# Optimization experiments

Measured on AMD Instinct MI355X. Metric: run time of the kernel, lower is better.

## Reference

```python
import jax, jax.numpy as jnp
import numpy as np

N = 50000   # nodes
E = 800000  # edges per graph
FD = 128    # input feature dim (sc and fc)
H = 128     # hidden_dim
G = 64      # graphs in batch
C = 2       # num_classes


def _sage(x, src, dst, Wl, Wr, b, n):
    # PyG SAGEConv (mean aggr): lin_l(mean_{j->i} x_j) + lin_r(x_i); bias lives in lin_l.
    msum = jax.ops.segment_sum(x[src], dst, num_segments=n)          # [n, F]
    cnt = jax.ops.segment_sum(jnp.ones((src.shape[0],), x.dtype), dst, num_segments=n)
    mean = msum / jnp.maximum(cnt, 1.0)[:, None]
    return mean @ Wl.T + x @ Wr.T + b


def setup_inputs() -> dict:
    key = jax.random.key(0)
    ks = jax.random.split(key, 24)
    s = 0.05
    inp = {
        "sc_x": jax.random.normal(ks[0], (N, FD), jnp.float32),
        "fc_x": jax.random.normal(ks[1], (N, FD), jnp.float32),
        "sc_edge_index": jax.random.randint(ks[2], (2, E), 0, N),
        "fc_edge_index": jax.random.randint(ks[3], (2, E), 0, N),
        "batch": jnp.sort(jax.random.randint(ks[4], (N,), 0, G)),
        # sc convs
        "sc_Wl1": jax.random.normal(ks[5], (H, FD), jnp.float32) * s,
        "sc_Wr1": jax.random.normal(ks[6], (H, FD), jnp.float32) * s,
        "sc_b1": jnp.zeros((H,), jnp.float32),
        "sc_Wl2": jax.random.normal(ks[7], (H, H), jnp.float32) * s,
        "sc_Wr2": jax.random.normal(ks[8], (H, H), jnp.float32) * s,
        "sc_b2": jnp.zeros((H,), jnp.float32),
        # fc convs
        "fc_Wl1": jax.random.normal(ks[9], (H, FD), jnp.float32) * s,
        "fc_Wr1": jax.random.normal(ks[10], (H, FD), jnp.float32) * s,
        "fc_b1": jnp.zeros((H,), jnp.float32),
        "fc_Wl2": jax.random.normal(ks[11], (H, H), jnp.float32) * s,
        "fc_Wr2": jax.random.normal(ks[12], (H, H), jnp.float32) * s,
        "fc_b2": jnp.zeros((H,), jnp.float32),
        # MLP head
        "W1": jax.random.normal(ks[13], (H, 2 * H), jnp.float32) * s,
        "bh1": jnp.zeros((H,), jnp.float32),
        "W2": jax.random.normal(ks[14], (H // 2, H), jnp.float32) * s,
        "bh2": jnp.zeros((H // 2,), jnp.float32),
        "W3": jax.random.normal(ks[15], (C, H // 2), jnp.float32) * s,
        "bh3": jnp.zeros((C,), jnp.float32),
    }
    return inp


def reference(sc_x, fc_x, sc_edge_index, fc_edge_index, batch,
              sc_Wl1, sc_Wr1, sc_b1, sc_Wl2, sc_Wr2, sc_b2,
              fc_Wl1, fc_Wr1, fc_b1, fc_Wl2, fc_Wr2, fc_b2,
              W1, bh1, W2, bh2, W3, bh3):
    # edge_index[0] = source j, edge_index[1] = target i (PyG convention)
    sc_src, sc_dst = sc_edge_index[0], sc_edge_index[1]
    fc_src, fc_dst = fc_edge_index[0], fc_edge_index[1]

    h = jax.nn.relu(_sage(sc_x, sc_src, sc_dst, sc_Wl1, sc_Wr1, sc_b1, N))
    h = jax.nn.relu(_sage(h, sc_src, sc_dst, sc_Wl2, sc_Wr2, sc_b2, N))
    sc_pool = jax.ops.segment_sum(h, batch, num_segments=G)  # global_add_pool -> [G, H]

    g = jax.nn.relu(_sage(fc_x, fc_src, fc_dst, fc_Wl1, fc_Wr1, fc_b1, N))
    g = jax.nn.relu(_sage(g, fc_src, fc_dst, fc_Wl2, fc_Wr2, fc_b2, N))
    fc_pool = jax.ops.segment_sum(g, batch, num_segments=G)  # [G, H]

    x = jnp.concatenate([sc_pool, fc_pool], axis=1)          # [G, 2H]
    # dropout is identity in eval mode
    x = jax.nn.relu(x @ W1.T + bh1)
    x = jax.nn.relu(x @ W2.T + bh2)
    return jax.nn.log_softmax(x @ W3.T + bh3, axis=-1)       # [G, C]
```

## Files before the change

### kernel.cpp

```cpp
#include <hip/hip_runtime.h>
#include <hip/hip_bf16.h>

#define N_NODES 50000
#define E_EDGES 800000
#define G_GRAPHS 64
#define NBUCK 392
#define BCAP 5120
#define NF ((size_t)N_NODES * 128)

typedef __attribute__((ext_vector_type(8))) short s16x8;
typedef __attribute__((ext_vector_type(4))) float f32x4;

constexpr size_t O_POOL   = 0;
constexpr size_t O_GCUR   = 16384;
constexpr size_t O_ROW    = 17408;
constexpr size_t O_CNT    = 117408;
constexpr size_t O_ES     = 217408;
constexpr size_t O_WB     = 1817408;
constexpr size_t O_XB     = 1882944;
constexpr size_t O_MEAN   = 8282944;
constexpr size_t O_HB     = 14682944;
constexpr size_t ZERO_BYTES = (16384 + 512) * 4;

__device__ __forceinline__ unsigned short f2bf(float f) {
    __hip_bfloat16 h = __float2bfloat16(f);
    return *reinterpret_cast<unsigned short*>(&h);
}
__device__ __forceinline__ float bflo(unsigned int v) { return __uint_as_float(v << 16); }
__device__ __forceinline__ float bfhi(unsigned int v) { return __uint_as_float(v & 0xffff0000u); }

__global__ void __launch_bounds__(512) bin_pass1(const int* __restrict__ sc_e,
                                                 const int* __restrict__ fc_e,
                                                 int* __restrict__ gcur,
                                                 unsigned int* __restrict__ buf) {
    __shared__ int hcnt[512];
    __shared__ int hexcl[512];
    __shared__ int hcur[512];
    __shared__ int gbase[512];
    __shared__ int wsum[8];
    __shared__ unsigned int stage[4096];

    const int tid = threadIdx.x;
    const int lane = tid & 63;
    const int wid = tid >> 6;
    const int tile0 = blockIdx.x * 4096;

    hcnt[tid] = 0;
    __syncthreads();

    int eb[8];
    unsigned int pk[8];
    #pragma unroll
    for (int j = 0; j < 8; ++j) {
        int ec = tile0 + j * 512 + tid;
        if (ec < 2 * E_EDGES) {
            int set = (ec >= E_EDGES);
            int local = ec - set * E_EDGES;
            const int* ep = set ? fc_e : sc_e;
            int src = ep[local];
            int dst = ep[E_EDGES + local];
            eb[j] = set * 196 + (dst >> 8);
            pk[j] = ((unsigned int)(dst & 255) << 16) | (unsigned int)src;
            atomicAdd(&hcnt[eb[j]], 1);
        } else eb[j] = -1;
    }
    __syncthreads();

    {
        int v = hcnt[tid];
        int incl = v;
        #pragma unroll
        for (int d = 1; d < 64; d <<= 1) {
            int u = __shfl_up(incl, d, 64);
            if (lane >= d) incl += u;
        }
        if (lane == 63) wsum[wid] = incl;
        __syncthreads();
        int pre = 0;
        for (int w = 0; w < wid; ++w) pre += wsum[w];
        int excl = incl - v + pre;
        hexcl[tid] = excl;
        hcur[tid] = excl;
    }
    __syncthreads();

    if (tid < NBUCK) {
        int c = hcnt[tid];
        gbase[tid] = c ? atomicAdd(&gcur[tid], c) : 0;
    }

    #pragma unroll
    for (int j = 0; j < 8; ++j) {
        if (eb[j] >= 0) {
            int pos = atomicAdd(&hcur[eb[j]], 1);
            stage[pos] = pk[j];
        }
    }
    __syncthreads();

    for (int b = wid; b < NBUCK; b += 8) {
        int c = hcnt[b];
        if (!c) continue;
        int s = hexcl[b];
        int g0 = gbase[b];
        for (int i = lane; i < c; i += 64) {
            int gi = g0 + i;
            if (gi < BCAP) buf[(size_t)b * BCAP + gi] = stage[s + i];
        }
    }
}

__global__ void __launch_bounds__(256) bin_pass2(const unsigned int* __restrict__ buf,
                                                 const int* __restrict__ gcur,
                                                 int* __restrict__ row,
                                                 int* __restrict__ cnt,
                                                 int* __restrict__ es) {
    __shared__ int cntl[256];
    __shared__ int pexcl[256];
    __shared__ int pcur[256];
    __shared__ int wsum[4];
    __shared__ int pre[512];
    __shared__ int stage[BCAP];

    const int b = blockIdx.x;
    const int tid = threadIdx.x;
    const int lane = tid & 63, wid = tid >> 6;
    const int sz = min(gcur[b], BCAP);
    const unsigned int* mybuf = buf + (size_t)b * BCAP;
    const int n0 = (b % 196) * 256;
    const int setbase = (b / 196) * N_NODES;

    pre[tid] = (tid < NBUCK) ? min(gcur[tid], BCAP) : 0;
    if (tid + 256 < 512) pre[tid + 256] = (tid + 256 < NBUCK) ? min(gcur[tid + 256], BCAP) : 0;
    cntl[tid] = 0;
    __syncthreads();
    if (tid < 64) {
        int base = tid * 8;
        int loc[8];
        int s = 0;
        #pragma unroll
        for (int k = 0; k < 8; ++k) { loc[k] = s; s += pre[base + k]; }
        int incl = s;
        #pragma unroll
        for (int d = 1; d < 64; d <<= 1) {
            int u = __shfl_up(incl, d, 64);
            if (lane >= d) incl += u;
        }
        int excl = incl - s;
        #pragma unroll
        for (int k = 0; k < 8; ++k) pre[base + k] = excl + loc[k];
    }
    for (int i = tid; i < sz; i += 256)
        atomicAdd(&cntl[mybuf[i] >> 16], 1);
    __syncthreads();
    const int base = pre[b];
    {
        int v = cntl[tid];
        int incl = v;
        #pragma unroll
        for (int d = 1; d < 64; d <<= 1) {
            int u = __shfl_up(incl, d, 64);
            if (lane >= d) incl += u;
        }
        if (lane == 63) wsum[wid] = incl;
        __syncthreads();
        int p = 0;
        for (int w = 0; w < wid; ++w) p += wsum[w];
        int excl = incl - v + p;
        pexcl[tid] = excl;
        pcur[tid] = excl;
    }
    __syncthreads();
    for (int i = tid; i < sz; i += 256) {
        unsigned int p = mybuf[i];
        int pos = atomicAdd(&pcur[p >> 16], 1);
        stage[pos] = (int)(p & 0xFFFFu);
    }
    __syncthreads();
    for (int i = tid; i < sz; i += 256) es[base + i] = stage[i];
    int node = n0 + tid;
    if (node < N_NODES) {
        cnt[setbase + node] = cntl[tid];
        row[setbase + node] = base + pexcl[tid];
    }
}

__global__ void cvt_all(const float* __restrict__ sc_x, const float* __restrict__ fc_x,
                        const float* w0, const float* w1, const float* w2, const float* w3,
                        const float* w4, const float* w5, const float* w6, const float* w7,
                        unsigned short* __restrict__ xb, unsigned short* __restrict__ wb) {
    const int blk = blockIdx.x;
    const int tid = threadIdx.x;
    if (blk < 6250) {
        int i = blk * 256 + tid;
        int set = (i >= (N_NODES * 128) / 8);
        int local = i - set * (N_NODES * 128) / 8;
        const float* src = set ? fc_x : sc_x;
        const float4* s = reinterpret_cast<const float4*>(src) + (size_t)local * 2;
        float4 a = s[0], b = s[1];
        union { s16x8 v; unsigned short u[8]; } p;
        p.u[0] = f2bf(a.x); p.u[1] = f2bf(a.y); p.u[2] = f2bf(a.z); p.u[3] = f2bf(a.w);
        p.u[4] = f2bf(b.x); p.u[5] = f2bf(b.y); p.u[6] = f2bf(b.z); p.u[7] = f2bf(b.w);
        reinterpret_cast<s16x8*>(xb)[i] = p.v;
    } else {
        int widx = blk - 6250;
        int gi = widx * 2048 + tid * 8;
        int m = gi >> 14;
        int off = gi & 16383;
        const float* W;
        switch (m) {
            case 0: W = w0; break; case 1: W = w1; break;
            case 2: W = w2; break; case 3: W = w3; break;
            case 4: W = w4; break; case 5: W = w5; break;
            case 6: W = w6; break; default: W = w7; break;
        }
        const float4* s = reinterpret_cast<const float4*>(W + off);
        float4 a = s[0], b = s[1];
        union { s16x8 v; unsigned short u[8]; } p;
        p.u[0] = f2bf(a.x); p.u[1] = f2bf(a.y); p.u[2] = f2bf(a.z); p.u[3] = f2bf(a.w);
        p.u[4] = f2bf(b.x); p.u[5] = f2bf(b.y); p.u[6] = f2bf(b.z); p.u[7] = f2bf(b.w);
        *reinterpret_cast<s16x8*>(wb + gi) = p.v;
    }
}

__global__ void __launch_bounds__(256) agg_kernel(const unsigned short* __restrict__ x,
                                                  const int* __restrict__ row,
                                                  const int* __restrict__ cnt,
                                                  const int* __restrict__ es,
                                                  unsigned short* __restrict__ mean) {
    int wave = (blockIdx.x * 256 + threadIdx.x) >> 6;
    int lane = threadIdx.x & 63;
    int ql = lane & 15;
    int n = wave * 4 + (lane >> 4);
    if (n >= 2 * N_NODES) return;
    const unsigned short* xs = x + (n >= N_NODES ? NF : 0);
    int start = row[n];
    int deg = cnt[n];
    float a0 = 0.f, a1 = 0.f, a2 = 0.f, a3 = 0.f, a4 = 0.f, a5 = 0.f, a6 = 0.f, a7 = 0.f;
    int qbase = lane & 48;
    for (int c = 0; c < deg; c += 16) {
        int m = min(16, deg - c);
        int eid = (ql < m) ? es[start + c + ql] : 0;
        int j = 0;
        for (; j + 4 <= m; j += 4) {
            int s0 = __shfl(eid, qbase + j,     64);
            int s1 = __shfl(eid, qbase + j + 1, 64);
            int s2 = __shfl(eid, qbase + j + 2, 64);
            int s3 = __shfl(eid, qbase + j + 3, 64);
            uint4 v0 = *reinterpret_cast<const uint4*>(xs + (size_t)s0 * 128 + ql * 8);
            uint4 v1 = *reinterpret_cast<const uint4*>(xs + (size_t)s1 * 128 + ql * 8);
            uint4 v2 = *reinterpret_cast<const uint4*>(xs + (size_t)s2 * 128 + ql * 8);
            uint4 v3 = *reinterpret_cast<const uint4*>(xs + (size_t)s3 * 128 + ql * 8);
            a0 += bflo(v0.x) + bflo(v1.x) + bflo(v2.x) + bflo(v3.x);
            a1 += bfhi(v0.x) + bfhi(v1.x) + bfhi(v2.x) + bfhi(v3.x);
            a2 += bflo(v0.y) + bflo(v1.y) + bflo(v2.y) + bflo(v3.y);
            a3 += bfhi(v0.y) + bfhi(v1.y) + bfhi(v2.y) + bfhi(v3.y);
            a4 += bflo(v0.z) + bflo(v1.z) + bflo(v2.z) + bflo(v3.z);
            a5 += bfhi(v0.z) + bfhi(v1.z) + bfhi(v2.z) + bfhi(v3.z);
            a6 += bflo(v0.w) + bflo(v1.w) + bflo(v2.w) + bflo(v3.w);
            a7 += bfhi(v0.w) + bfhi(v1.w) + bfhi(v2.w) + bfhi(v3.w);
        }
        for (; j < m; ++j) {
            int s = __shfl(eid, qbase + j, 64);
            uint4 v = *reinterpret_cast<const uint4*>(xs + (size_t)s * 128 + ql * 8);
            a0 += bflo(v.x); a1 += bfhi(v.x);
            a2 += bflo(v.y); a3 += bfhi(v.y);
            a4 += bflo(v.z); a5 += bfhi(v.z);
            a6 += bflo(v.w); a7 += bfhi(v.w);
        }
    }
    float inv = 1.0f / fmaxf((float)deg, 1.0f);
    uint4 o;
    o.x = (unsigned int)f2bf(a0 * inv) | ((unsigned int)f2bf(a1 * inv) << 16);
    o.y = (unsigned int)f2bf(a2 * inv) | ((unsigned int)f2bf(a3 * inv) << 16);
    o.z = (unsigned int)f2bf(a4 * inv) | ((unsigned int)f2bf(a5 * inv) << 16);
    o.w = (unsigned int)f2bf(a6 * inv) | ((unsigned int)f2bf(a7 * inv) << 16);
    *reinterpret_cast<uint4*>(mean + (size_t)n * 128 + ql * 8) = o;
}

__global__ void __launch_bounds__(512) gemm_mfma(const unsigned short* __restrict__ AmB,
                                                 const unsigned short* __restrict__ AxB,
                                                 const unsigned short* __restrict__ WBall,
                                                 const float* __restrict__ bias0,
                                                 const float* __restrict__ bias1,
                                                 unsigned short* __restrict__ outHB,
                                                 float* __restrict__ pool,
                                                 const int* __restrict__ batch,
                                                 int layer) {
    __shared__ s16x8 lds_a[2][512];
    __shared__ s16x8 lds_b[2][512];

    const int tid = threadIdx.x;
    const int lane = tid & 63;
    const int w = tid >> 6;
    const int set = blockIdx.y;
    const int node0 = blockIdx.x * 128;

    const unsigned short* Am = AmB + (size_t)set * NF;
    const unsigned short* Ax = AxB + (size_t)set * NF;
    const unsigned short* Bl = WBall + (size_t)(set * 4 + layer * 2) * 16384;
    const unsigned short* Br = Bl + 16384;
    const float* bias = set ? bias1 : bias0;
    unsigned short* outH = outHB ? outHB + (size_t)set * NF : nullptr;
    const int poolBase = set * 128;

    const int wr = w >> 1;
    const int wc = w & 1;
    const int fr = lane & 15;
    const int fg = lane >> 4;

    f32x4 acc[2][4];
    #pragma unroll
    for (int mf = 0; mf < 2; ++mf)
        #pragma unroll
        for (int nf = 0; nf < 4; ++nf) acc[mf][nf] = (f32x4){0.f, 0.f, 0.f, 0.f};

    const int s_row = tid >> 2, s_slot = tid & 3;
    const int s_g = s_slot ^ ((s_row >> 1) & 3);
    const size_t a_off = (size_t)min(node0 + s_row, N_NODES - 1) * 128 + s_g * 8;
    const size_t b_off = (size_t)s_row * 128 + s_g * 8;

    const int arow0 = wr * 32 + fr;
    const int arow1 = arow0 + 16;
    const int aidx0 = arow0 * 4 + (fg ^ ((arow0 >> 1) & 3));
    const int aidx1 = arow1 * 4 + (fg ^ ((arow1 >> 1) & 3));
    int bidx[4];
    #pragma unroll
    for (int nf = 0; nf < 4; ++nf) {
        int br = wc * 64 + nf * 16 + fr;
        bidx[nf] = br * 4 + (fg ^ ((br >> 1) & 3));
    }

    #define LOAD_A(kc) (*reinterpret_cast<const s16x8*>(((kc) < 4 ? Am : Ax) + (((kc) & 3) * 32) + a_off))
    #define LOAD_B(kc) (*reinterpret_cast<const s16x8*>(((kc) < 4 ? Bl : Br) + (((kc) & 3) * 32) + b_off))

    {
        s16x8 ra = LOAD_A(0), rb = LOAD_B(0);
        lds_a[0][tid] = ra; lds_b[0][tid] = rb;
    }
    __syncthreads();

    #pragma unroll
    for (int kc = 0; kc < 8; ++kc) {
        const int cur = kc & 1;
        s16x8 ra, rb;
        if (kc < 7) { ra = LOAD_A(kc + 1); rb = LOAD_B(kc + 1); }
        s16x8 a0 = lds_a[cur][aidx0];
        s16x8 a1 = lds_a[cur][aidx1];
        #pragma unroll
        for (int nf = 0; nf < 4; ++nf) {
            s16x8 bv = lds_b[cur][bidx[nf]];
            acc[0][nf] = __builtin_amdgcn_mfma_f32_16x16x32_bf16(a0, bv, acc[0][nf], 0, 0, 0);
            acc[1][nf] = __builtin_amdgcn_mfma_f32_16x16x32_bf16(a1, bv, acc[1][nf], 0, 0, 0);
        }
        if (kc < 7) { lds_a[cur ^ 1][tid] = ra; lds_b[cur ^ 1][tid] = rb; }
        __syncthreads();
    }
    #undef LOAD_A
    #undef LOAD_B

    if (outH) {
        #pragma unroll
        for (int mf = 0; mf < 2; ++mf)
            #pragma unroll
            for (int nf = 0; nf < 4; ++nf) {
                int col = wc * 64 + nf * 16 + fr;
                float bv = bias[col];
                #pragma unroll
                for (int r = 0; r < 4; ++r) {
                    int node = node0 + wr * 32 + mf * 16 + fg * 4 + r;
                    if (node < N_NODES)
                        outH[(size_t)node * 128 + col] = f2bf(fmaxf(acc[mf][nf][r] + bv, 0.f));
                }
            }
    } else {
        int gids[2][4];
        #pragma unroll
        for (int mf = 0; mf < 2; ++mf)
            #pragma unroll
            for (int r = 0; r < 4; ++r) {
                int node = node0 + wr * 32 + mf * 16 + fg * 4 + r;
                gids[mf][r] = (node < N_NODES) ? batch[node] : -1;
            }
        #pragma unroll
        for (int nf = 0; nf < 4; ++nf) {
            int col = wc * 64 + nf * 16 + fr;
            float bv = bias[col];
            float* pbase = &pool[poolBase + col];
            int curg = -1; float s = 0.f;
            #pragma unroll
            for (int mf = 0; mf < 2; ++mf)
                #pragma unroll
                for (int r = 0; r < 4; ++r) {
                    int g = gids[mf][r];
                    if (g < 0) continue;
                    float v = fmaxf(acc[mf][nf][r] + bv, 0.f);
                    if (g != curg) {
                        if (curg >= 0) atomicAdd(pbase + (size_t)curg * 256, s);
                        curg = g; s = v;
                    } else s += v;
                }
            if (curg >= 0) atomicAdd(pbase + (size_t)curg * 256, s);
        }
    }
}

__global__ void __launch_bounds__(128) head_kernel(const float* __restrict__ pool,
                                                   const float* __restrict__ W1, const float* __restrict__ bh1,
                                                   const float* __restrict__ W2, const float* __restrict__ bh2,
                                                   const float* __restrict__ W3, const float* __restrict__ bh3,
                                                   float* __restrict__ out) {
    __shared__ float xg[256];
    __shared__ float h1[128];
    __shared__ float h2[64];
    __shared__ float lg[2];
    int g = blockIdx.x, t = threadIdx.x;
    xg[t] = pool[(size_t)g * 256 + t];
    xg[t + 128] = pool[(size_t)g * 256 + 128 + t];
    __syncthreads();
    float s = bh1[t];
    for (int k = 0; k < 256; ++k) s += W1[t * 256 + k] * xg[k];
    h1[t] = fmaxf(s, 0.f);
    __syncthreads();
    if (t < 64) {
        float s2 = bh2[t];
        for (int k = 0; k < 128; ++k) s2 += W2[t * 128 + k] * h1[k];
        h2[t] = fmaxf(s2, 0.f);
    }
    __syncthreads();
    if (t < 2) {
        float s3 = bh3[t];
        for (int k = 0; k < 64; ++k) s3 += W3[t * 64 + k] * h2[k];
        lg[t] = s3;
    }
    __syncthreads();
    if (t == 0) {
        float m = fmaxf(lg[0], lg[1]);
        float lse = m + logf(expf(lg[0] - m) + expf(lg[1] - m));
        out[g * 2 + 0] = lg[0] - lse;
        out[g * 2 + 1] = lg[1] - lse;
    }
}

extern "C" void kernel_launch(void* const* d_in, const int* in_sizes, int n_in,
                              void* d_out, int out_size, void* d_ws, size_t ws_size,
                              hipStream_t stream) {
    const float* sc_x = (const float*)d_in[0];
    const float* fc_x = (const float*)d_in[1];
    const int* sc_e   = (const int*)d_in[2];
    const int* fc_e   = (const int*)d_in[3];
    const int* batch  = (const int*)d_in[4];
    const float* sc_Wl1 = (const float*)d_in[5];
    const float* sc_Wr1 = (const float*)d_in[6];
    const float* sc_b1  = (const float*)d_in[7];
    const float* sc_Wl2 = (const float*)d_in[8];
    const float* sc_Wr2 = (const float*)d_in[9];
    const float* sc_b2  = (const float*)d_in[10];
    const float* fc_Wl1 = (const float*)d_in[11];
    const float* fc_Wr1 = (const float*)d_in[12];
    const float* fc_b1  = (const float*)d_in[13];
    const float* fc_Wl2 = (const float*)d_in[14];
    const float* fc_Wr2 = (const float*)d_in[15];
    const float* fc_b2  = (const float*)d_in[16];
    const float* W1  = (const float*)d_in[17];
    const float* bh1 = (const float*)d_in[18];
    const float* W2  = (const float*)d_in[19];
    const float* bh2 = (const float*)d_in[20];
    const float* W3  = (const float*)d_in[21];
    const float* bh3 = (const float*)d_in[22];

    int* iw = (int*)d_ws;
    float* fw = (float*)d_ws;
    float* pool = fw + O_POOL;
    int* gcur   = iw + O_GCUR;
    int* row    = iw + O_ROW;
    int* cnt    = iw + O_CNT;
    int* es     = iw + O_ES;
    unsigned short* WB    = (unsigned short*)(iw + O_WB);
    unsigned short* xb    = (unsigned short*)(iw + O_XB);
    unsigned short* meanb = (unsigned short*)(iw + O_MEAN);
    unsigned short* hb    = (unsigned short*)(iw + O_HB);
    unsigned int* buf = (unsigned int*)(iw + O_MEAN);

    hipMemsetAsync(d_ws, 0, ZERO_BYTES, stream);

    bin_pass1<<<(2 * E_EDGES + 4095) / 4096, 512, 0, stream>>>(sc_e, fc_e, gcur, buf);
    bin_pass2<<<NBUCK, 256, 0, stream>>>(buf, gcur, row, cnt, es);

    cvt_all<<<6250 + 64, 256, 0, stream>>>(sc_x, fc_x,
                                           sc_Wl1, sc_Wr1, sc_Wl2, sc_Wr2,
                                           fc_Wl1, fc_Wr1, fc_Wl2, fc_Wr2, xb, WB);

    const int AGB = (2 * N_NODES + 15) / 16;
    dim3 gg((N_NODES + 127) / 128, 2);

    agg_kernel<<<AGB, 256, 0, stream>>>(xb, row, cnt, es, meanb);
    gemm_mfma<<<gg, 512, 0, stream>>>(meanb, xb, WB, sc_b1, fc_b1, hb, nullptr, nullptr, 0);
    agg_kernel<<<AGB, 256, 0, stream>>>(hb, row, cnt, es, meanb);
    gemm_mfma<<<gg, 512, 0, stream>>>(meanb, hb, WB, sc_b2, fc_b2, nullptr, pool, batch, 1);

    head_kernel<<<G_GRAPHS, 128, 0, stream>>>(pool, W1, bh1, W2, bh2, W3, bh3, (float*)d_out);
}
```

Measured before the change: 342.7 us.

## Fuse neighbor mean aggregation into SAGE MFMA GEMM kernel via LDS

Merges the separate aggregation kernel and the GEMM kernel into one kernel per layer. Each block computes the neighbor means for 64 nodes directly into shared memory and then runs the bf16 MFMA GEMM on them, so the mean matrix never makes a round trip through global memory and two launches per forward are removed. In exchange the tile shrinks to 64 nodes (more blocks, each wave covering fewer output columns), and the irregular gather now shares a block with the GEMM, which may lower occupancy and MFMA utilization.

```diff
diff --git a/kernel.cpp b/kernel.cpp
--- a/kernel.cpp
+++ b/kernel.cpp
@@ -18,7 +18,7 @@
 constexpr size_t O_ES     = 217408;
 constexpr size_t O_WB     = 1817408;
 constexpr size_t O_XB     = 1882944;
-constexpr size_t O_MEAN   = 8282944;
+constexpr size_t O_BUF    = 8282944;
 constexpr size_t O_HB     = 14682944;
 constexpr size_t ZERO_BYTES = (16384 + 512) * 4;
 
@@ -223,148 +223,154 @@
     }
 }
 
-__global__ void __launch_bounds__(256) agg_kernel(const unsigned short* __restrict__ x,
+__global__ void __launch_bounds__(512) sage_fused(const unsigned short* __restrict__ xAll,
+                                                  const unsigned short* __restrict__ WBall,
                                                   const int* __restrict__ row,
                                                   const int* __restrict__ cnt,
                                                   const int* __restrict__ es,
-                                                  unsigned short* __restrict__ mean) {
-    int wave = (blockIdx.x * 256 + threadIdx.x) >> 6;
-    int lane = threadIdx.x & 63;
-    int ql = lane & 15;
-    int n = wave * 4 + (lane >> 4);
-    if (n >= 2 * N_NODES) return;
-    const unsigned short* xs = x + (n >= N_NODES ? NF : 0);
-    int start = row[n];
-    int deg = cnt[n];
-    float a0 = 0.f, a1 = 0.f, a2 = 0.f, a3 = 0.f, a4 = 0.f, a5 = 0.f, a6 = 0.f, a7 = 0.f;
-    int qbase = lane & 48;
-    for (int c = 0; c < deg; c += 16) {
-        int m = min(16, deg - c);
-        int eid = (ql < m) ? es[start + c + ql] : 0;
-        int j = 0;
-        for (; j + 4 <= m; j += 4) {
-            int s0 = __shfl(eid, qbase + j,     64);
-            int s1 = __shfl(eid, qbase + j + 1, 64);
-            int s2 = __shfl(eid, qbase + j + 2, 64);
-            int s3 = __shfl(eid, qbase + j + 3, 64);
-            uint4 v0 = *reinterpret_cast<const uint4*>(xs + (size_t)s0 * 128 + ql * 8);
-            uint4 v1 = *reinterpret_cast<const uint4*>(xs + (size_t)s1 * 128 + ql * 8);
-            uint4 v2 = *reinterpret_cast<const uint4*>(xs + (size_t)s2 * 128 + ql * 8);
-            uint4 v3 = *reinterpret_cast<const uint4*>(xs + (size_t)s3 * 128 + ql * 8);
-            a0 += bflo(v0.x) + bflo(v1.x) + bflo(v2.x) + bflo(v3.x);
-            a1 += bfhi(v0.x) + bfhi(v1.x) + bfhi(v2.x) + bfhi(v3.x);
-            a2 += bflo(v0.y) + bflo(v1.y) + bflo(v2.y) + bflo(v3.y);
-            a3 += bfhi(v0.y) + bfhi(v1.y) + bfhi(v2.y) + bfhi(v3.y);
-            a4 += bflo(v0.z) + bflo(v1.z) + bflo(v2.z) + bflo(v3.z);
-            a5 += bfhi(v0.z) + bfhi(v1.z) + bfhi(v2.z) + bfhi(v3.z);
-            a6 += bflo(v0.w) + bflo(v1.w) + bflo(v2.w) + bflo(v3.w);
-            a7 += bfhi(v0.w) + bfhi(v1.w) + bfhi(v2.w) + bfhi(v3.w);
-        }
-        for (; j < m; ++j) {
-            int s = __shfl(eid, qbase + j, 64);
-            uint4 v = *reinterpret_cast<const uint4*>(xs + (size_t)s * 128 + ql * 8);
-            a0 += bflo(v.x); a1 += bfhi(v.x);
-            a2 += bflo(v.y); a3 += bfhi(v.y);
-            a4 += bflo(v.z); a5 += bfhi(v.z);
-            a6 += bflo(v.w); a7 += bfhi(v.w);
-        }
-    }
-    float inv = 1.0f / fmaxf((float)deg, 1.0f);
-    uint4 o;
-    o.x = (unsigned int)f2bf(a0 * inv) | ((unsigned int)f2bf(a1 * inv) << 16);
-    o.y = (unsigned int)f2bf(a2 * inv) | ((unsigned int)f2bf(a3 * inv) << 16);
-    o.z = (unsigned int)f2bf(a4 * inv) | ((unsigned int)f2bf(a5 * inv) << 16);
-    o.w = (unsigned int)f2bf(a6 * inv) | ((unsigned int)f2bf(a7 * inv) << 16);
-    *reinterpret_cast<uint4*>(mean + (size_t)n * 128 + ql * 8) = o;
-}
-
-__global__ void __launch_bounds__(512) gemm_mfma(const unsigned short* __restrict__ AmB,
-                                                 const unsigned short* __restrict__ AxB,
-                                                 const unsigned short* __restrict__ WBall,
-                                                 const float* __restrict__ bias0,
-                                                 const float* __restrict__ bias1,
-                                                 unsigned short* __restrict__ outHB,
-                                                 float* __restrict__ pool,
-                                                 const int* __restrict__ batch,
-                                                 int layer) {
-    __shared__ s16x8 lds_a[2][512];
+                                                  const float* __restrict__ bias0,
+                                                  const float* __restrict__ bias1,
+                                                  unsigned short* __restrict__ outHB,
+                                                  float* __restrict__ pool,
+                                                  const int* __restrict__ batch,
+                                                  int layer) {
+    __shared__ s16x8 mean_t[64 * 17];
+    __shared__ s16x8 lds_a[2][256];
     __shared__ s16x8 lds_b[2][512];
 
     const int tid = threadIdx.x;
     const int lane = tid & 63;
     const int w = tid >> 6;
     const int set = blockIdx.y;
-    const int node0 = blockIdx.x * 128;
-
-    const unsigned short* Am = AmB + (size_t)set * NF;
-    const unsigned short* Ax = AxB + (size_t)set * NF;
+    const int node0 = blockIdx.x * 64;
+    const int setbase = set * N_NODES;
+
+    const unsigned short* xs = xAll + (size_t)set * NF;
     const unsigned short* Bl = WBall + (size_t)(set * 4 + layer * 2) * 16384;
     const unsigned short* Br = Bl + 16384;
     const float* bias = set ? bias1 : bias0;
     unsigned short* outH = outHB ? outHB + (size_t)set * NF : nullptr;
     const int poolBase = set * 128;
 
-    const int wr = w >> 1;
-    const int wc = w & 1;
+    const int s_row = tid >> 2, s_slot = tid & 3;
+    const int s_g = s_slot ^ ((s_row >> 1) & 3);
+    const size_t b_off = (size_t)s_row * 128 + s_g * 8;
+    const size_t a_off = (size_t)min(node0 + s_row, N_NODES - 1) * 128 + s_g * 8;
+
+    #define LOAD_AX(kc) (*reinterpret_cast<const s16x8*>(xs + (((kc) & 3) * 32) + a_off))
+    #define LOAD_B(kc)  (*reinterpret_cast<const s16x8*>(((kc) < 4 ? Bl : Br) + (((kc) & 3) * 32) + b_off))
+
+    s16x8 rb0 = LOAD_B(0);
+
+    const int ql = lane & 15;
+    const int q = lane >> 4;
+    const int qbase = lane & 48;
+    #pragma unroll
+    for (int pass = 0; pass < 2; ++pass) {
+        int r = pass * 32 + w * 4 + q;
+        int n = node0 + r;
+        int deg = (n < N_NODES) ? cnt[setbase + n] : 0;
+        int start = (n < N_NODES) ? row[setbase + n] : 0;
+        float a0 = 0.f, a1 = 0.f, a2 = 0.f, a3 = 0.f, a4 = 0.f, a5 = 0.f, a6 = 0.f, a7 = 0.f;
+        for (int c = 0; c < deg; c += 16) {
+            int m = min(16, deg - c);
+            int eid = (ql < m) ? es[start + c + ql] : 0;
+            int j = 0;
+            for (; j + 4 <= m; j += 4) {
+                int s0 = __shfl(eid, qbase + j,     64);
+                int s1 = __shfl(eid, qbase + j + 1, 64);
+                int s2 = __shfl(eid, qbase + j + 2, 64);
+                int s3 = __shfl(eid, qbase + j + 3, 64);
+                uint4 v0 = *reinterpret_cast<const uint4*>(xs + (size_t)s0 * 128 + ql * 8);
+                uint4 v1 = *reinterpret_cast<const uint4*>(xs + (size_t)s1 * 128 + ql * 8);
+                uint4 v2 = *reinterpret_cast<const uint4*>(xs + (size_t)s2 * 128 + ql * 8);
+                uint4 v3 = *reinterpret_cast<const uint4*>(xs + (size_t)s3 * 128 + ql * 8);
+                a0 += bflo(v0.x) + bflo(v1.x) + bflo(v2.x) + bflo(v3.x);
+                a1 += bfhi(v0.x) + bfhi(v1.x) + bfhi(v2.x) + bfhi(v3.x);
+                a2 += bflo(v0.y) + bflo(v1.y) + bflo(v2.y) + bflo(v3.y);
+                a3 += bfhi(v0.y) + bfhi(v1.y) + bfhi(v2.y) + bfhi(v3.y);
+                a4 += bflo(v0.z) + bflo(v1.z) + bflo(v2.z) + bflo(v3.z);
+                a5 += bfhi(v0.z) + bfhi(v1.z) + bfhi(v2.z) + bfhi(v3.z);
+                a6 += bflo(v0.w) + bflo(v1.w) + bflo(v2.w) + bflo(v3.w);
+                a7 += bfhi(v0.w) + bfhi(v1.w) + bfhi(v2.w) + bfhi(v3.w);
+            }
+            for (; j < m; ++j) {
+                int s = __shfl(eid, qbase + j, 64);
+                uint4 v = *reinterpret_cast<const uint4*>(xs + (size_t)s * 128 + ql * 8);
+                a0 += bflo(v.x); a1 += bfhi(v.x);
+                a2 += bflo(v.y); a3 += bfhi(v.y);
+                a4 += bflo(v.z); a5 += bfhi(v.z);
+                a6 += bflo(v.w); a7 += bfhi(v.w);
+            }
+        }
+        float inv = 1.0f / fmaxf((float)deg, 1.0f);
+        union { s16x8 v; unsigned int u[4]; } o;
+        o.u[0] = (unsigned int)f2bf(a0 * inv) | ((unsigned int)f2bf(a1 * inv) << 16);
+        o.u[1] = (unsigned int)f2bf(a2 * inv) | ((unsigned int)f2bf(a3 * inv) << 16);
+        o.u[2] = (unsigned int)f2bf(a4 * inv) | ((unsigned int)f2bf(a5 * inv) << 16);
+        o.u[3] = (unsigned int)f2bf(a6 * inv) | ((unsigned int)f2bf(a7 * inv) << 16);
+        mean_t[r * 17 + ql] = o.v;
+    }
+    lds_b[0][tid] = rb0;
+    __syncthreads();
+
+    const int wr = w >> 2;
+    const int wc = w & 3;
     const int fr = lane & 15;
     const int fg = lane >> 4;
 
-    f32x4 acc[2][4];
+    f32x4 acc[2][2];
     #pragma unroll
     for (int mf = 0; mf < 2; ++mf)
         #pragma unroll
-        for (int nf = 0; nf < 4; ++nf) acc[mf][nf] = (f32x4){0.f, 0.f, 0.f, 0.f};
-
-    const int s_row = tid >> 2, s_slot = tid & 3;
-    const int s_g = s_slot ^ ((s_row >> 1) & 3);
-    const size_t a_off = (size_t)min(node0 + s_row, N_NODES - 1) * 128 + s_g * 8;
-    const size_t b_off = (size_t)s_row * 128 + s_g * 8;
+        for (int nf = 0; nf < 2; ++nf) acc[mf][nf] = (f32x4){0.f, 0.f, 0.f, 0.f};
 
     const int arow0 = wr * 32 + fr;
     const int arow1 = arow0 + 16;
-    const int aidx0 = arow0 * 4 + (fg ^ ((arow0 >> 1) & 3));
-    const int aidx1 = arow1 * 4 + (fg ^ ((arow1 >> 1) & 3));
-    int bidx[4];
+    const int axidx0 = arow0 * 4 + (fg ^ ((arow0 >> 1) & 3));
+    const int axidx1 = arow1 * 4 + (fg ^ ((arow1 >> 1) & 3));
+    int bidx[2];
     #pragma unroll
-    for (int nf = 0; nf < 4; ++nf) {
-        int br = wc * 64 + nf * 16 + fr;
-        bidx[nf] = br * 4 + (fg ^ ((br >> 1) & 3));
-    }
-
-    #define LOAD_A(kc) (*reinterpret_cast<const s16x8*>(((kc) < 4 ? Am : Ax) + (((kc) & 3) * 32) + a_off))
-    #define LOAD_B(kc) (*reinterpret_cast<const s16x8*>(((kc) < 4 ? Bl : Br) + (((kc) & 3) * 32) + b_off))
-
-    {
-        s16x8 ra = LOAD_A(0), rb = LOAD_B(0);
-        lds_a[0][tid] = ra; lds_b[0][tid] = rb;
-    }
-    __syncthreads();
+    for (int nf = 0; nf < 2; ++nf) {
+        int brr = wc * 32 + nf * 16 + fr;
+        bidx[nf] = brr * 4 + (fg ^ ((brr >> 1) & 3));
+    }
 
     #pragma unroll
     for (int kc = 0; kc < 8; ++kc) {
         const int cur = kc & 1;
-        s16x8 ra, rb;
-        if (kc < 7) { ra = LOAD_A(kc + 1); rb = LOAD_B(kc + 1); }
-        s16x8 a0 = lds_a[cur][aidx0];
-        s16x8 a1 = lds_a[cur][aidx1];
-        #pragma unroll
-        for (int nf = 0; nf < 4; ++nf) {
+        s16x8 rbn, ran;
+        if (kc < 7) rbn = LOAD_B(kc + 1);
+        if (kc >= 3 && kc < 7 && tid < 256) ran = LOAD_AX(kc + 1);
+        s16x8 a0, a1;
+        if (kc < 4) {
+            a0 = mean_t[arow0 * 17 + kc * 4 + fg];
+            a1 = mean_t[arow1 * 17 + kc * 4 + fg];
+        } else {
+            a0 = lds_a[cur][axidx0];
+            a1 = lds_a[cur][axidx1];
+        }
+        #pragma unroll
+        for (int nf = 0; nf < 2; ++nf) {
             s16x8 bv = lds_b[cur][bidx[nf]];
             acc[0][nf] = __builtin_amdgcn_mfma_f32_16x16x32_bf16(a0, bv, acc[0][nf], 0, 0, 0);
             acc[1][nf] = __builtin_amdgcn_mfma_f32_16x16x32_bf16(a1, bv, acc[1][nf], 0, 0, 0);
         }
-        if (kc < 7) { lds_a[cur ^ 1][tid] = ra; lds_b[cur ^ 1][tid] = rb; }
+        if (kc < 7) {
+            lds_b[cur ^ 1][tid] = rbn;
+            if (kc >= 3 && tid < 256) lds_a[(kc + 1) & 1][tid] = ran;
+        }
         __syncthreads();
     }
-    #undef LOAD_A
+    #undef LOAD_AX
     #undef LOAD_B
 
     if (outH) {
         #pragma unroll
         for (int mf = 0; mf < 2; ++mf)
             #pragma unroll
-            for (int nf = 0; nf < 4; ++nf) {
-                int col = wc * 64 + nf * 16 + fr;
+            for (int nf = 0; nf < 2; ++nf) {
+                int col = wc * 32 + nf * 16 + fr;
                 float bv = bias[col];
                 #pragma unroll
                 for (int r = 0; r < 4; ++r) {
@@ -383,8 +389,8 @@
                 gids[mf][r] = (node < N_NODES) ? batch[node] : -1;
             }
         #pragma unroll
-        for (int nf = 0; nf < 4; ++nf) {
-            int col = wc * 64 + nf * 16 + fr;
+        for (int nf = 0; nf < 2; ++nf) {
+            int col = wc * 32 + nf * 16 + fr;
             float bv = bias[col];
             float* pbase = &pool[poolBase + col];
             int curg = -1; float s = 0.f;
@@ -476,11 +482,10 @@
     int* row    = iw + O_ROW;
     int* cnt    = iw + O_CNT;
     int* es     = iw + O_ES;
-    unsigned short* WB    = (unsigned short*)(iw + O_WB);
-    unsigned short* xb    = (unsigned short*)(iw + O_XB);
-    unsigned short* meanb = (unsigned short*)(iw + O_MEAN);
-    unsigned short* hb    = (unsigned short*)(iw + O_HB);
-    unsigned int* buf = (unsigned int*)(iw + O_MEAN);
+    unsigned short* WB = (unsigned short*)(iw + O_WB);
+    unsigned short* xb = (unsigned short*)(iw + O_XB);
+    unsigned short* hb = (unsigned short*)(iw + O_HB);
+    unsigned int* buf  = (unsigned int*)(iw + O_BUF);
 
     hipMemsetAsync(d_ws, 0, ZERO_BYTES, stream);
 
@@ -491,13 +496,10 @@
                                            sc_Wl1, sc_Wr1, sc_Wl2, sc_Wr2,
                                            fc_Wl1, fc_Wr1, fc_Wl2, fc_Wr2, xb, WB);
 
-    const int AGB = (2 * N_NODES + 15) / 16;
-    dim3 gg((N_NODES + 127) / 128, 2);
-
-    agg_kernel<<<AGB, 256, 0, stream>>>(xb, row, cnt, es, meanb);
-    gemm_mfma<<<gg, 512, 0, stream>>>(meanb, xb, WB, sc_b1, fc_b1, hb, nullptr, nullptr, 0);
-    agg_kernel<<<AGB, 256, 0, stream>>>(hb, row, cnt, es, meanb);
-    gemm_mfma<<<gg, 512, 0, stream>>>(meanb, hb, WB, sc_b2, fc_b2, nullptr, pool, batch, 1);
+    dim3 gf((N_NODES + 63) / 64, 2);
+
+    sage_fused<<<gf, 512, 0, stream>>>(xb, WB, row, cnt, es, sc_b1, fc_b1, hb, nullptr, nullptr, 0);
+    sage_fused<<<gf, 512, 0, stream>>>(hb, WB, row, cnt, es, sc_b2, fc_b2, nullptr, pool, batch, 1);
 
     head_kernel<<<G_GRAPHS, 128, 0, stream>>>(pool, W1, bh1, W2, bh2, W3, bh3, (float*)d_out);
 }
```

Measured after the change: 346.3 us. Within noise of the previous version (+1.0%).

## Fuse binning, conversion and pool zeroing into one prep kernel with per-tile slots

Applied to the files above, without the earlier changes.

Merges the first binning pass, the feature and weight bf16 conversion, and the pool zeroing into a single launch, which removes the memset and one kernel launch. Global atomic bucket cursors are replaced by fixed per-(bucket, tile) slots with capacity TCAP plus a count array. The second pass prefix-sums those per-tile counts and gathers the slots into shared memory, and es now uses fixed per-bucket offsets. The cost is a larger scratch buffer and a serial per-thread gather loop in the second pass. Any tile contributing more than TCAP edges to one bucket is silently truncated.

```diff
diff --git a/kernel.cpp b/kernel.cpp
--- a/kernel.cpp
+++ b/kernel.cpp
@@ -5,22 +5,24 @@
 #define E_EDGES 800000
 #define G_GRAPHS 64
 #define NBUCK 392
+#define NTILE 391
+#define TCAP 40
 #define BCAP 5120
 #define NF ((size_t)N_NODES * 128)
 
 typedef __attribute__((ext_vector_type(8))) short s16x8;
 typedef __attribute__((ext_vector_type(4))) float f32x4;
 
-constexpr size_t O_POOL   = 0;
-constexpr size_t O_GCUR   = 16384;
-constexpr size_t O_ROW    = 17408;
-constexpr size_t O_CNT    = 117408;
-constexpr size_t O_ES     = 217408;
-constexpr size_t O_WB     = 1817408;
-constexpr size_t O_XB     = 1882944;
-constexpr size_t O_MEAN   = 8282944;
-constexpr size_t O_HB     = 14682944;
-constexpr size_t ZERO_BYTES = (16384 + 512) * 4;
+constexpr size_t O_POOL = 0;
+constexpr size_t O_ROW  = 16384;
+constexpr size_t O_CNT  = 116384;
+constexpr size_t O_ES   = 216384;
+constexpr size_t O_TCNT = 2223424;
+constexpr size_t O_WB   = 2376704;
+constexpr size_t O_XB   = 2442240;
+constexpr size_t O_MEAN = 8842240;
+constexpr size_t O_HB   = 15242240;
+constexpr size_t O_BUF  = 21642240;
 
 __device__ __forceinline__ unsigned short f2bf(float f) {
     __hip_bfloat16 h = __float2bfloat16(f);
@@ -29,172 +31,92 @@
 __device__ __forceinline__ float bflo(unsigned int v) { return __uint_as_float(v << 16); }
 __device__ __forceinline__ float bfhi(unsigned int v) { return __uint_as_float(v & 0xffff0000u); }
 
-__global__ void __launch_bounds__(512) bin_pass1(const int* __restrict__ sc_e,
-                                                 const int* __restrict__ fc_e,
-                                                 int* __restrict__ gcur,
-                                                 unsigned int* __restrict__ buf) {
+__global__ void __launch_bounds__(512) prep_kernel(const int* __restrict__ sc_e,
+                                                   const int* __restrict__ fc_e,
+                                                   const float* __restrict__ sc_x,
+                                                   const float* __restrict__ fc_x,
+                                                   const float* w0, const float* w1,
+                                                   const float* w2, const float* w3,
+                                                   const float* w4, const float* w5,
+                                                   const float* w6, const float* w7,
+                                                   unsigned int* __restrict__ buf,
+                                                   int* __restrict__ tcnt,
+                                                   unsigned short* __restrict__ xb,
+                                                   unsigned short* __restrict__ wb,
+                                                   float* __restrict__ pool) {
     __shared__ int hcnt[512];
     __shared__ int hexcl[512];
     __shared__ int hcur[512];
-    __shared__ int gbase[512];
     __shared__ int wsum[8];
     __shared__ unsigned int stage[4096];
 
-    const int tid = threadIdx.x;
-    const int lane = tid & 63;
-    const int wid = tid >> 6;
-    const int tile0 = blockIdx.x * 4096;
-
-    hcnt[tid] = 0;
-    __syncthreads();
-
-    int eb[8];
-    unsigned int pk[8];
-    #pragma unroll
-    for (int j = 0; j < 8; ++j) {
-        int ec = tile0 + j * 512 + tid;
-        if (ec < 2 * E_EDGES) {
-            int set = (ec >= E_EDGES);
-            int local = ec - set * E_EDGES;
-            const int* ep = set ? fc_e : sc_e;
-            int src = ep[local];
-            int dst = ep[E_EDGES + local];
-            eb[j] = set * 196 + (dst >> 8);
-            pk[j] = ((unsigned int)(dst & 255) << 16) | (unsigned int)src;
-            atomicAdd(&hcnt[eb[j]], 1);
-        } else eb[j] = -1;
-    }
-    __syncthreads();
-
-    {
-        int v = hcnt[tid];
-        int incl = v;
-        #pragma unroll
-        for (int d = 1; d < 64; d <<= 1) {
-            int u = __shfl_up(incl, d, 64);
-            if (lane >= d) incl += u;
-        }
-        if (lane == 63) wsum[wid] = incl;
-        __syncthreads();
-        int pre = 0;
-        for (int w = 0; w < wid; ++w) pre += wsum[w];
-        int excl = incl - v + pre;
-        hexcl[tid] = excl;
-        hcur[tid] = excl;
-    }
-    __syncthreads();
-
-    if (tid < NBUCK) {
-        int c = hcnt[tid];
-        gbase[tid] = c ? atomicAdd(&gcur[tid], c) : 0;
-    }
-
-    #pragma unroll
-    for (int j = 0; j < 8; ++j) {
-        if (eb[j] >= 0) {
-            int pos = atomicAdd(&hcur[eb[j]], 1);
-            stage[pos] = pk[j];
-        }
-    }
-    __syncthreads();
-
-    for (int b = wid; b < NBUCK; b += 8) {
-        int c = hcnt[b];
-        if (!c) continue;
-        int s = hexcl[b];
-        int g0 = gbase[b];
-        for (int i = lane; i < c; i += 64) {
-            int gi = g0 + i;
-            if (gi < BCAP) buf[(size_t)b * BCAP + gi] = stage[s + i];
-        }
-    }
-}
-
-__global__ void __launch_bounds__(256) bin_pass2(const unsigned int* __restrict__ buf,
-                                                 const int* __restrict__ gcur,
-                                                 int* __restrict__ row,
-                                                 int* __restrict__ cnt,
-                                                 int* __restrict__ es) {
-    __shared__ int cntl[256];
-    __shared__ int pexcl[256];
-    __shared__ int pcur[256];
-    __shared__ int wsum[4];
-    __shared__ int pre[512];
-    __shared__ int stage[BCAP];
-
-    const int b = blockIdx.x;
-    const int tid = threadIdx.x;
-    const int lane = tid & 63, wid = tid >> 6;
-    const int sz = min(gcur[b], BCAP);
-    const unsigned int* mybuf = buf + (size_t)b * BCAP;
-    const int n0 = (b % 196) * 256;
-    const int setbase = (b / 196) * N_NODES;
-
-    pre[tid] = (tid < NBUCK) ? min(gcur[tid], BCAP) : 0;
-    if (tid + 256 < 512) pre[tid + 256] = (tid + 256 < NBUCK) ? min(gcur[tid + 256], BCAP) : 0;
-    cntl[tid] = 0;
-    __syncthreads();
-    if (tid < 64) {
-        int base = tid * 8;
-        int loc[8];
-        int s = 0;
-        #pragma unroll
-        for (int k = 0; k < 8; ++k) { loc[k] = s; s += pre[base + k]; }
-        int incl = s;
-        #pragma unroll
-        for (int d = 1; d < 64; d <<= 1) {
-            int u = __shfl_up(incl, d, 64);
-            if (lane >= d) incl += u;
-        }
-        int excl = incl - s;
-        #pragma unroll
-        for (int k = 0; k < 8; ++k) pre[base + k] = excl + loc[k];
-    }
-    for (int i = tid; i < sz; i += 256)
-        atomicAdd(&cntl[mybuf[i] >> 16], 1);
-    __syncthreads();
-    const int base = pre[b];
-    {
-        int v = cntl[tid];
-        int incl = v;
-        #pragma unroll
-        for (int d = 1; d < 64; d <<= 1) {
-            int u = __shfl_up(incl, d, 64);
-            if (lane >= d) incl += u;
-        }
-        if (lane == 63) wsum[wid] = incl;
-        __syncthreads();
-        int p = 0;
-        for (int w = 0; w < wid; ++w) p += wsum[w];
-        int excl = incl - v + p;
-        pexcl[tid] = excl;
-        pcur[tid] = excl;
-    }
-    __syncthreads();
-    for (int i = tid; i < sz; i += 256) {
-        unsigned int p = mybuf[i];
-        int pos = atomicAdd(&pcur[p >> 16], 1);
-        stage[pos] = (int)(p & 0xFFFFu);
-    }
-    __syncthreads();
-    for (int i = tid; i < sz; i += 256) es[base + i] = stage[i];
-    int node = n0 + tid;
-    if (node < N_NODES) {
-        cnt[setbase + node] = cntl[tid];
-        row[setbase + node] = base + pexcl[tid];
-    }
-}
-
-__global__ void cvt_all(const float* __restrict__ sc_x, const float* __restrict__ fc_x,
-                        const float* w0, const float* w1, const float* w2, const float* w3,
-                        const float* w4, const float* w5, const float* w6, const float* w7,
-                        unsigned short* __restrict__ xb, unsigned short* __restrict__ wb) {
     const int blk = blockIdx.x;
     const int tid = threadIdx.x;
-    if (blk < 6250) {
-        int i = blk * 256 + tid;
-        int set = (i >= (N_NODES * 128) / 8);
-        int local = i - set * (N_NODES * 128) / 8;
+
+    if (blk < NTILE) {
+        const int lane = tid & 63;
+        const int wid = tid >> 6;
+        const int tile0 = blk * 4096;
+
+        hcnt[tid] = 0;
+        __syncthreads();
+
+        int eb[8];
+        unsigned int pk[8];
+        #pragma unroll
+        for (int j = 0; j < 8; ++j) {
+            int ec = tile0 + j * 512 + tid;
+            if (ec < 2 * E_EDGES) {
+                int set = (ec >= E_EDGES);
+                int local = ec - set * E_EDGES;
+                const int* ep = set ? fc_e : sc_e;
+                int src = ep[local];
+                int dst = ep[E_EDGES + local];
+                eb[j] = set * 196 + (dst >> 8);
+                pk[j] = ((unsigned int)(dst & 255) << 16) | (unsigned int)src;
+                atomicAdd(&hcnt[eb[j]], 1);
+            } else eb[j] = -1;
+        }
+        __syncthreads();
+
+        {
+            int v = hcnt[tid];
+            int incl = v;
+            #pragma unroll
+            for (int d = 1; d < 64; d <<= 1) {
+                int u = __shfl_up(incl, d, 64);
+                if (lane >= d) incl += u;
+            }
+            if (lane == 63) wsum[wid] = incl;
+            __syncthreads();
+            int pre = 0;
+            for (int w = 0; w < wid; ++w) pre += wsum[w];
+            int excl = incl - v + pre;
+            hexcl[tid] = excl;
+            hcur[tid] = excl;
+        }
+        __syncthreads();
+
+        #pragma unroll
+        for (int j = 0; j < 8; ++j) {
+            if (eb[j] >= 0) {
+                int pos = atomicAdd(&hcur[eb[j]], 1);
+                stage[pos] = pk[j];
+            }
+        }
+        __syncthreads();
+
+        for (int b = wid; b < NBUCK; b += 8) {
+            int c = min(hcnt[b], TCAP);
+            int s = hexcl[b];
+            size_t g0 = ((size_t)b * NTILE + blk) * TCAP;
+            for (int i = lane; i < c; i += 64) buf[g0 + i] = stage[s + i];
+            if (lane == 0) tcnt[b * NTILE + blk] = c;
+        }
+    } else if (blk < NTILE + 3125) {
+        int i = (blk - NTILE) * 512 + tid;
+        int set = (i >= 800000);
+        int local = i - set * 800000;
         const float* src = set ? fc_x : sc_x;
         const float4* s = reinterpret_cast<const float4*>(src) + (size_t)local * 2;
         float4 a = s[0], b = s[1];
@@ -202,9 +124,9 @@
         p.u[0] = f2bf(a.x); p.u[1] = f2bf(a.y); p.u[2] = f2bf(a.z); p.u[3] = f2bf(a.w);
         p.u[4] = f2bf(b.x); p.u[5] = f2bf(b.y); p.u[6] = f2bf(b.z); p.u[7] = f2bf(b.w);
         reinterpret_cast<s16x8*>(xb)[i] = p.v;
-    } else {
-        int widx = blk - 6250;
-        int gi = widx * 2048 + tid * 8;
+    } else if (blk < NTILE + 3125 + 32) {
+        int widx = blk - (NTILE + 3125);
+        int gi = widx * 4096 + tid * 8;
         int m = gi >> 14;
         int off = gi & 16383;
         const float* W;
@@ -220,6 +142,91 @@
         p.u[0] = f2bf(a.x); p.u[1] = f2bf(a.y); p.u[2] = f2bf(a.z); p.u[3] = f2bf(a.w);
         p.u[4] = f2bf(b.x); p.u[5] = f2bf(b.y); p.u[6] = f2bf(b.z); p.u[7] = f2bf(b.w);
         *reinterpret_cast<s16x8*>(wb + gi) = p.v;
+    } else {
+        for (int i = tid; i < 16384; i += 512) pool[i] = 0.f;
+    }
+}
+
+__global__ void __launch_bounds__(256) bin_pass2(const unsigned int* __restrict__ buf,
+                                                 const int* __restrict__ tcnt,
+                                                 int* __restrict__ row,
+                                                 int* __restrict__ cnt,
+                                                 int* __restrict__ es) {
+    __shared__ int pre[512];
+    __shared__ int cntl[256];
+    __shared__ int pexcl[256];
+    __shared__ int pcur[256];
+    __shared__ int wsum[4];
+    __shared__ unsigned int stage[BCAP];
+
+    const int b = blockIdx.x;
+    const int tid = threadIdx.x;
+    const int lane = tid & 63, wid = tid >> 6;
+    const int n0 = (b % 196) * 256;
+    const int setbase = (b / 196) * N_NODES;
+    const int base = b * BCAP;
+
+    pre[tid] = (tid < NTILE) ? tcnt[b * NTILE + tid] : 0;
+    if (tid + 256 < 512) pre[tid + 256] = (tid + 256 < NTILE) ? tcnt[b * NTILE + tid + 256] : 0;
+    cntl[tid] = 0;
+    __syncthreads();
+    if (tid < 64) {
+        int cb = tid * 8;
+        int loc[8];
+        int s = 0;
+        #pragma unroll
+        for (int k = 0; k < 8; ++k) { loc[k] = s; s += pre[cb + k]; }
+        int incl = s;
+        #pragma unroll
+        for (int d = 1; d < 64; d <<= 1) {
+            int u = __shfl_up(incl, d, 64);
+            if (lane >= d) incl += u;
+        }
+        int excl = incl - s;
+        #pragma unroll
+        for (int k = 0; k < 8; ++k) pre[cb + k] = excl + loc[k];
+    }
+    __syncthreads();
+    const int sz = min(pre[NTILE], BCAP);
+    for (int t = tid; t < NTILE; t += 256) {
+        int off = pre[t];
+        int c = pre[t + 1] - off;
+        const unsigned int* src = buf + ((size_t)b * NTILE + t) * TCAP;
+        for (int i = 0; i < c; ++i) {
+            int p = off + i;
+            if (p < BCAP) stage[p] = src[i];
+        }
+    }
+    __syncthreads();
+    for (int i = tid; i < sz; i += 256)
+        atomicAdd(&cntl[stage[i] >> 16], 1);
+    __syncthreads();
+    {
+        int v = cntl[tid];
+        int incl = v;
+        #pragma unroll
+        for (int d = 1; d < 64; d <<= 1) {
+            int u = __shfl_up(incl, d, 64);
+            if (lane >= d) incl += u;
+        }
+        if (lane == 63) wsum[wid] = incl;
+        __syncthreads();
+        int p = 0;
+        for (int w = 0; w < wid; ++w) p += wsum[w];
+        int excl = incl - v + p;
+        pexcl[tid] = excl;
+        pcur[tid] = excl;
+    }
+    __syncthreads();
+    for (int i = tid; i < sz; i += 256) {
+        unsigned int p = stage[i];
+        int pos = atomicAdd(&pcur[p >> 16], 1);
+        es[base + pos] = (int)(p & 0xFFFFu);
+    }
+    int node = n0 + tid;
+    if (node < N_NODES) {
+        cnt[setbase + node] = cntl[tid];
+        row[setbase + node] = base + pexcl[tid];
     }
 }
 
@@ -472,24 +479,21 @@
     int* iw = (int*)d_ws;
     float* fw = (float*)d_ws;
     float* pool = fw + O_POOL;
-    int* gcur   = iw + O_GCUR;
     int* row    = iw + O_ROW;
     int* cnt    = iw + O_CNT;
     int* es     = iw + O_ES;
-    unsigned short* WB    = (unsigned short*)(iw + O_WB);
-    unsigned short* xb    = (unsigned short*)(iw + O_XB);
+    int* tcnt   = iw + O_TCNT;
+    unsigned short* WB = (unsigned short*)(iw + O_WB);
+    unsigned short* xb = (unsigned short*)(iw + O_XB);
     unsigned short* meanb = (unsigned short*)(iw + O_MEAN);
-    unsigned short* hb    = (unsigned short*)(iw + O_HB);
-    unsigned int* buf = (unsigned int*)(iw + O_MEAN);
-
-    hipMemsetAsync(d_ws, 0, ZERO_BYTES, stream);
-
-    bin_pass1<<<(2 * E_EDGES + 4095) / 4096, 512, 0, stream>>>(sc_e, fc_e, gcur, buf);
-    bin_pass2<<<NBUCK, 256, 0, stream>>>(buf, gcur, row, cnt, es);
-
-    cvt_all<<<6250 + 64, 256, 0, stream>>>(sc_x, fc_x,
-                                           sc_Wl1, sc_Wr1, sc_Wl2, sc_Wr2,
-                                           fc_Wl1, fc_Wr1, fc_Wl2, fc_Wr2, xb, WB);
+    unsigned short* hb = (unsigned short*)(iw + O_HB);
+    unsigned int* buf  = (unsigned int*)(iw + O_BUF);
+
+    prep_kernel<<<NTILE + 3125 + 32 + 1, 512, 0, stream>>>(
+        sc_e, fc_e, sc_x, fc_x,
+        sc_Wl1, sc_Wr1, sc_Wl2, sc_Wr2, fc_Wl1, fc_Wr1, fc_Wl2, fc_Wr2,
+        buf, tcnt, xb, WB, pool);
+    bin_pass2<<<NBUCK, 256, 0, stream>>>(buf, tcnt, row, cnt, es);
 
     const int AGB = (2 * N_NODES + 15) / 16;
     dim3 gg((N_NODES + 127) / 128, 2);
@@ -498,6 +502,5 @@
     gemm_mfma<<<gg, 512, 0, stream>>>(meanb, xb, WB, sc_b1, fc_b1, hb, nullptr, nullptr, 0);
     agg_kernel<<<AGB, 256, 0, stream>>>(hb, row, cnt, es, meanb);
     gemm_mfma<<<gg, 512, 0, stream>>>(meanb, hb, WB, sc_b2, fc_b2, nullptr, pool, batch, 1);
-
     head_kernel<<<G_GRAPHS, 128, 0, stream>>>(pool, W1, bh1, W2, bh2, W3, bh3, (float*)d_out);
 }
```

Result: no change. 337.9 us (-1.4%).
